# Kernel tuning notes

Measured on AMD Instinct MI355X. Metric: run time of the kernel, lower is better.

Reference implementation:

```python
import jax, jax.numpy as jnp
import numpy as np

N = 50000      # nodes per type
E = 800000     # edges per type (avg degree 16)
D = 128        # feature dim == hidden_channels
L = 3          # num_layers
G = 16         # graphs in batch
OUT = 2


def setup_inputs() -> dict:
    key = jax.random.key(0)
    ks = jax.random.split(key, 12)
    return {
        "x_void": jax.random.normal(ks[0], (N, D), jnp.float32),
        "x_vessel": jax.random.normal(ks[1], (N, D), jnp.float32),
        "Wl": jax.random.normal(ks[2], (L, 2, D, D), jnp.float32) * 0.05,
        "bl": jax.random.normal(ks[3], (L, 2, D), jnp.float32) * 0.05,
        "Wr": jax.random.normal(ks[4], (L, 2, D, D), jnp.float32) * 0.05,
        "lin_W": jax.random.normal(ks[5], (2 * D, OUT), jnp.float32) * 0.05,
        "lin_b": jax.random.normal(ks[6], (OUT,), jnp.float32) * 0.05,
        "edge_void": jax.random.randint(ks[7], (2, E), 0, N, jnp.int64 if jax.config.jax_enable_x64 else jnp.int32),
        "edge_vessel": jax.random.randint(ks[8], (2, E), 0, N, jnp.int64 if jax.config.jax_enable_x64 else jnp.int32),
        "batch_void": jnp.sort(jax.random.randint(ks[9], (N,), 0, G)),
        "batch_vessel": jnp.sort(jax.random.randint(ks[10], (N,), 0, G)),
    }


def _sage(x, src, dst, Wl_t, bl_t, Wr_t):
    # PyG SAGEConv (aggr='mean'): lin_l(mean_{j in N(i)} x_j) + lin_r(x_i)
    n = x.shape[0]
    agg = jax.ops.segment_sum(x[src], dst, num_segments=n)  # [n, D]
    cnt = jax.ops.segment_sum(jnp.ones((src.shape[0],), x.dtype), dst, num_segments=n)
    mean = agg / jnp.maximum(cnt, 1.0)[:, None]
    return mean @ Wl_t + bl_t + x @ Wr_t


def _mean_pool(x, batch, num_graphs):
    s = jax.ops.segment_sum(x, batch, num_segments=num_graphs)
    c = jax.ops.segment_sum(jnp.ones((x.shape[0],), x.dtype), batch, num_segments=num_graphs)
    return s / jnp.maximum(c, 1.0)[:, None]


def reference(x_void, x_vessel, Wl, bl, Wr, lin_W, lin_b,
              edge_void, edge_vessel, batch_void, batch_vessel):
    xs = [x_void, x_vessel]
    edges = [edge_void, edge_vessel]
    for l in range(L):
        xs = [jax.nn.relu(_sage(xs[t], edges[t][0], edges[t][1], Wl[l, t], bl[l, t], Wr[l, t]))
              for t in range(2)]
    reps = [_mean_pool(xs[0], batch_void, G), _mean_pool(xs[1], batch_vessel, G)]
    h = jnp.concatenate(reps, axis=1)  # [G, 2D]; dropout inactive (training=False)
    return h @ lin_W + lin_b
```

## Files before the change

kernel.cpp:

```cpp
#include <hip/hip_runtime.h>
#include <hip/hip_bf16.h>
#include <cstdint>
#include <cstddef>

static constexpr int FD = 128;
static constexpr int NG = 16;
static constexpr int NL = 3;

typedef __attribute__((ext_vector_type(8))) short short8;
typedef __attribute__((ext_vector_type(4))) float floatx4;

__device__ __forceinline__ short f2bf(float v) {
  union { __hip_bfloat16 b; short s; } u;
  u.b = __float2bfloat16(v);
  return u.s;
}
__device__ __forceinline__ float bfu(unsigned short u) {
  return __uint_as_float((unsigned int)u << 16);
}

__global__ __launch_bounds__(256) void k_bucket(
    const int* __restrict__ e0, const int* __restrict__ e1,
    int* __restrict__ gcount, int* __restrict__ buckets,
    int E, int NBUCK, int CAP)
{
  __shared__ int hist[256], lexcl[256], gbase[256], wcur[256];
  __shared__ int staged[4096];
  __shared__ int wsum[4];
  __shared__ int totalS;
  int tid = (int)threadIdx.x;
  int bx = (int)blockIdx.x;
  int t = bx & 1;
  int chunk = (bx >> 1) * 4096;
  const int* eg = t ? e1 : e0;
  hist[tid] = 0;
  __syncthreads();
  unsigned int ent[16];
  #pragma unroll
  for (int k = 0; k < 16; k++) {
    int i = chunk + k * 256 + tid;
    if (i < E) {
      unsigned int src = (unsigned int)eg[i];
      unsigned int dst = (unsigned int)eg[E + i];
      ent[k] = src | (dst << 16);
      atomicAdd(&hist[dst >> 8], 1);
    } else ent[k] = 0xFFFFFFFFu;
  }
  __syncthreads();
  int lane = tid & 63, wv = tid >> 6;
  int v = hist[tid];
  int sc = v;
  #pragma unroll
  for (int d = 1; d < 64; d <<= 1) {
    int tt = __shfl_up(sc, d, 64);
    if (lane >= d) sc += tt;
  }
  if (lane == 63) wsum[wv] = sc;
  __syncthreads();
  int wpre = 0;
  for (int w = 0; w < wv; w++) wpre += wsum[w];
  int excl = wpre + sc - v;
  lexcl[tid] = excl;
  wcur[tid] = excl;
  gbase[tid] = v ? atomicAdd(&gcount[t * 256 + tid], v) : 0;
  if (tid == 255) totalS = excl + v;
  __syncthreads();
  #pragma unroll
  for (int k = 0; k < 16; k++) {
    if (ent[k] != 0xFFFFFFFFu) {
      int b = ent[k] >> 24;
      int pos = atomicAdd(&wcur[b], 1);
      staged[pos] = (int)ent[k];
    }
  }
  __syncthreads();
  int total = totalS;
  for (int j = tid; j < total; j += 256) {
    unsigned int e = (unsigned int)staged[j];
    int b = e >> 24;
    int gp = gbase[b] + (j - lexcl[b]);
    if (gp < CAP) buckets[((size_t)t * NBUCK + b) * CAP + gp] = (int)e;
  }
}

__global__ __launch_bounds__(256) void k_csr(
    const int* __restrict__ gcount, const int* __restrict__ buckets,
    int* __restrict__ csr0, int* __restrict__ csr1,
    int* __restrict__ off0, int* __restrict__ off1,
    int* __restrict__ deg0, int* __restrict__ deg1,
    int NBUCK, int CAP, int n)
{
  __shared__ int hist[256], wcur[256], wsum[4];
  int tid = (int)threadIdx.x;
  int bx = (int)blockIdx.x;
  int t = bx & 1;
  int b = bx >> 1;
  int cnt = gcount[t * 256 + b];
  if (cnt > CAP) cnt = CAP;
  const int* base = buckets + ((size_t)t * NBUCK + b) * CAP;
  int* csr = t ? csr1 : csr0;
  int* off = t ? off1 : off0;
  int* deg = t ? deg1 : deg0;
  hist[tid] = 0;
  __syncthreads();
  for (int j = tid; j < cnt; j += 256)
    atomicAdd(&hist[((unsigned int)base[j] >> 16) & 255], 1);
  __syncthreads();
  int lane = tid & 63, wv = tid >> 6;
  int v = hist[tid];
  int sc = v;
  #pragma unroll
  for (int d = 1; d < 64; d <<= 1) {
    int tt = __shfl_up(sc, d, 64);
    if (lane >= d) sc += tt;
  }
  if (lane == 63) wsum[wv] = sc;
  __syncthreads();
  int wpre = 0;
  for (int w = 0; w < wv; w++) wpre += wsum[w];
  int excl = wpre + sc - v;
  wcur[tid] = excl;
  int node = b * 256 + tid;
  if (node < n) { deg[node] = v; off[node] = b * CAP + excl; }
  __syncthreads();
  for (int j = tid; j < cnt; j += 256) {
    unsigned int e = (unsigned int)base[j];
    int ld = (e >> 16) & 255;
    int pos = atomicAdd(&wcur[ld], 1);
    csr[b * CAP + pos] = (int)(e & 0xFFFFu);
  }
}

__global__ void k_wconv(const float* __restrict__ Wl, const float* __restrict__ Wr,
                        short* __restrict__ Wf) {
  int u = blockIdx.x * blockDim.x + threadIdx.x;
  if (u >= 6 * 8192) return;
  int combo = u >> 13;
  int r = u & 8191;
  int l  = r & 63;
  int nt = (r >> 6) & 7;
  int h  = (r >> 9) & 1;
  int ks = r >> 10;
  short8 s;
  #pragma unroll
  for (int j = 0; j < 8; j++) {
    int k = ks * 32 + (l >> 4) * 8 + j;
    int n = nt * 16 + (l & 15);
    float w = (k < FD) ? Wl[((size_t)combo * FD + k) * FD + n]
                       : Wr[((size_t)combo * FD + (k - FD)) * FD + n];
    __hip_bfloat16 hb = __float2bfloat16(w);
    if (h == 0) {
      union { __hip_bfloat16 b; short t; } uu; uu.b = hb; s[j] = uu.t;
    } else {
      float hf = __bfloat162float(hb);
      s[j] = f2bf(w - hf);
    }
  }
  *(short8*)(Wf + (size_t)combo * 65536 + (size_t)r * 8) = s;
}

__global__ __launch_bounds__(256) void k_xconv(
    const float* __restrict__ x0, const float* __restrict__ x1,
    short* __restrict__ a0, short* __restrict__ a1,
    short* __restrict__ r0, short* __restrict__ r1, int n) {
  int bx = blockIdx.x;
  int t = bx & 1;
  int g = bx >> 1;
  const float* x = t ? x1 : x0;
  short* a = t ? a1 : a0;
  short* rm = t ? r1 : r0;
  int tid = (int)threadIdx.x;
  int m = tid & 15;
  int kb = tid >> 4;
  int node = g * 16 + m;
  if (node >= n) return;
  const float* src = x + (size_t)node * FD + kb * 8;
  short8 s;
  #pragma unroll
  for (int j = 0; j < 8; j++) s[j] = f2bf(src[j]);
  *(short8*)(a + (size_t)g * 2048 + kb * 128 + m * 8) = s;
  *(short8*)(rm + (size_t)node * FD + kb * 8) = s;
}

__global__ __launch_bounds__(512) void k_agg(
    const unsigned short* __restrict__ x0, const unsigned short* __restrict__ x1,
    const int* __restrict__ csr0, const int* __restrict__ csr1,
    const int* __restrict__ off0, const int* __restrict__ off1,
    const int* __restrict__ deg0, const int* __restrict__ deg1,
    short* __restrict__ m0, short* __restrict__ m1, int n)
{
  __shared__ float M[16][132];
  int bx = blockIdx.x;
  int t = bx & 1;
  int g = bx >> 1;
  const unsigned short* x = t ? x1 : x0;
  const int* csr  = t ? csr1 : csr0;
  const int* off  = t ? off1 : off0;
  const int* deg  = t ? deg1 : deg0;
  short* mAF      = t ? m1 : m0;
  int tid = (int)threadIdx.x;
  int s = tid >> 5;
  int tx = tid & 31;
  int c4 = tx * 4;
  int node = g * 16 + s;
  if (node < n) {
    int o = off[node], d = deg[node];
    float a0 = 0.f, a1 = 0.f, a2 = 0.f, a3 = 0.f;
    for (int k0 = 0; k0 < d; k0 += 32) {
      int idx = (k0 + tx < d) ? csr[o + k0 + tx] : 0;
      int mm = min(32, d - k0);
      int j = 0;
      for (; j + 8 <= mm; j += 8) {
        int s0 = __shfl(idx, j + 0, 32);
        int s1 = __shfl(idx, j + 1, 32);
        int s2 = __shfl(idx, j + 2, 32);
        int s3 = __shfl(idx, j + 3, 32);
        int s4 = __shfl(idx, j + 4, 32);
        int s5 = __shfl(idx, j + 5, 32);
        int s6 = __shfl(idx, j + 6, 32);
        int s7 = __shfl(idx, j + 7, 32);
        ushort4 u0 = *(const ushort4*)&x[(size_t)s0 * FD + c4];
        ushort4 u1 = *(const ushort4*)&x[(size_t)s1 * FD + c4];
        ushort4 u2 = *(const ushort4*)&x[(size_t)s2 * FD + c4];
        ushort4 u3 = *(const ushort4*)&x[(size_t)s3 * FD + c4];
        ushort4 u4 = *(const ushort4*)&x[(size_t)s4 * FD + c4];
        ushort4 u5 = *(const ushort4*)&x[(size_t)s5 * FD + c4];
        ushort4 u6 = *(const ushort4*)&x[(size_t)s6 * FD + c4];
        ushort4 u7 = *(const ushort4*)&x[(size_t)s7 * FD + c4];
        a0 += ((bfu(u0.x) + bfu(u1.x)) + (bfu(u2.x) + bfu(u3.x)))
            + ((bfu(u4.x) + bfu(u5.x)) + (bfu(u6.x) + bfu(u7.x)));
        a1 += ((bfu(u0.y) + bfu(u1.y)) + (bfu(u2.y) + bfu(u3.y)))
            + ((bfu(u4.y) + bfu(u5.y)) + (bfu(u6.y) + bfu(u7.y)));
        a2 += ((bfu(u0.z) + bfu(u1.z)) + (bfu(u2.z) + bfu(u3.z)))
            + ((bfu(u4.z) + bfu(u5.z)) + (bfu(u6.z) + bfu(u7.z)));
        a3 += ((bfu(u0.w) + bfu(u1.w)) + (bfu(u2.w) + bfu(u3.w)))
            + ((bfu(u4.w) + bfu(u5.w)) + (bfu(u6.w) + bfu(u7.w)));
      }
      for (; j < mm; j++) {
        int si = __shfl(idx, j, 32);
        ushort4 u = *(const ushort4*)&x[(size_t)si * FD + c4];
        a0 += bfu(u.x); a1 += bfu(u.y); a2 += bfu(u.z); a3 += bfu(u.w);
      }
    }
    float inv = 1.f / fmaxf((float)d, 1.f);
    M[s][c4 + 0] = a0 * inv;
    M[s][c4 + 1] = a1 * inv;
    M[s][c4 + 2] = a2 * inv;
    M[s][c4 + 3] = a3 * inv;
  }
  __syncthreads();
  if (tid < 256) {
    int m = tid & 15;
    int kb = tid >> 4;
    if (g * 16 + m < n) {
      short8 v;
      #pragma unroll
      for (int j = 0; j < 8; j++) v[j] = f2bf(M[m][kb * 8 + j]);
      *(short8*)(mAF + (size_t)g * 2048 + kb * 128 + m * 8) = v;
    }
  }
}

__global__ __launch_bounds__(256) void k_gemm(
    const short* __restrict__ mAF0, const short* __restrict__ mAF1,
    const short* __restrict__ xAF0, const short* __restrict__ xAF1,
    const short* __restrict__ Wf,
    const float* __restrict__ bl,
    short* __restrict__ obf0, short* __restrict__ obf1,
    short* __restrict__ oAF0, short* __restrict__ oAF1, int n)
{
  __shared__ __align__(16) char smem[32768];
  short* WfL = (short*)smem;
  float* S   = (float*)smem;

  int tid = (int)threadIdx.x;
  int l = tid & 63;
  int wv = tid >> 6;
  int bx = (int)blockIdx.x;
  int t = bx & 1;
  int tile = bx >> 1;
  int row0 = tile * 128;
  int g0 = tile * 8;

  const short* mAF = t ? mAF1 : mAF0;
  const short* xAF = t ? xAF1 : xAF0;
  const short* Wc  = Wf + (size_t)t * 65536;
  const float* bias = bl + t * FD;
  short* obf = t ? obf1 : obf0;
  short* oAF = t ? oAF1 : oAF0;

  int rhalf = wv & 1;
  int chalf = wv >> 1;
  int laneoff = (l >> 4) * 128 + (l & 15) * 8;

  auto stageW = [&](int ks, int buf) {
    const short* src = Wc + ks * 8192 + wv * 2048;
    short* dst = WfL + buf * 8192 + wv * 2048;
    #pragma unroll
    for (int i = 0; i < 4; i++) {
      __builtin_amdgcn_global_load_lds(
          (const __attribute__((address_space(1))) void*)(src + i * 512 + l * 8),
          (__attribute__((address_space(3))) void*)(dst + i * 512),
          16, 0, 0);
    }
  };

  floatx4 acc[4][4];
  #pragma unroll
  for (int i = 0; i < 4; i++)
    #pragma unroll
    for (int q = 0; q < 4; q++) acc[i][q] = (floatx4)0.f;

  short8 Acur[4], Anext[4];
  auto loadA = [&](int ks, short8* A) {
    const short* Ab = (ks < 4 ? mAF : xAF) + (ks & 3) * 512;
    #pragma unroll
    for (int i = 0; i < 4; i++) {
      int g = g0 + rhalf * 4 + i;
      A[i] = *(const short8*)(Ab + (size_t)g * 2048 + laneoff);
    }
  };

  stageW(0, 0);
  loadA(0, Acur);
  for (int ks = 0; ks < 8; ks++) {
    int buf = ks & 1;
    __syncthreads();
    if (ks < 7) { stageW(ks + 1, buf ^ 1); loadA(ks + 1, Anext); }
    const short* WB = WfL + buf * 8192;
    #pragma unroll
    for (int q = 0; q < 4; q++) {
      int nt = chalf * 4 + q;
      short8 whi = *(const short8*)(WB + nt * 512 + l * 8);
      short8 wlo = *(const short8*)(WB + 4096 + nt * 512 + l * 8);
      #pragma unroll
      for (int i = 0; i < 4; i++) {
        acc[i][q] = __builtin_amdgcn_mfma_f32_16x16x32_bf16(Acur[i], whi, acc[i][q], 0, 0, 0);
        acc[i][q] = __builtin_amdgcn_mfma_f32_16x16x32_bf16(Acur[i], wlo, acc[i][q], 0, 0, 0);
      }
    }
    #pragma unroll
    for (int i = 0; i < 4; i++) Acur[i] = Anext[i];
  }

  #pragma unroll
  for (int q = 0; q < 4; q++) {
    int col = chalf * 64 + q * 16 + (l & 15);
    float b = bias[col];
    #pragma unroll
    for (int i = 0; i < 4; i++)
      #pragma unroll
      for (int r = 0; r < 4; r++)
        acc[i][q][r] = fmaxf(acc[i][q][r] + b, 0.f);
  }

  #pragma unroll
  for (int ph = 0; ph < 2; ph++) {
    __syncthreads();
    if (chalf == ph) {
      #pragma unroll
      for (int i = 0; i < 4; i++)
        #pragma unroll
        for (int q = 0; q < 4; q++)
          #pragma unroll
          for (int r = 0; r < 4; r++)
            S[(rhalf * 64 + i * 16 + (l >> 4) * 4 + r) * 64 + q * 16 + (l & 15)] = acc[i][q][r];
    }
    __syncthreads();
    #pragma unroll
    for (int it = 0; it < 4; it++) {
      int u = it * 256 + tid;
      int m = u & 15;
      int kb = (u >> 4) & 7;
      int grp = u >> 7;
      int rl = grp * 16 + m;
      if (row0 + rl < n) {
        short8 s;
        #pragma unroll
        for (int j = 0; j < 8; j++) s[j] = f2bf(S[rl * 64 + kb * 8 + j]);
        *(short8*)(oAF + (size_t)(g0 + grp) * 2048 + (ph * 8 + kb) * 128 + m * 8) = s;
        *(short8*)(obf + (size_t)(row0 + rl) * FD + ph * 64 + kb * 8) = s;
      }
    }
  }
}

__global__ __launch_bounds__(256) void k_pool(
    const unsigned short* __restrict__ x0, const unsigned short* __restrict__ x1,
    const int* __restrict__ b0, const int* __restrict__ b1,
    float* __restrict__ pool, float* __restrict__ pcnt, int n) {
  int bx = (int)blockIdx.x;
  int t = bx & 1;
  const unsigned short* x = t ? x1 : x0;
  const int* batch = t ? b1 : b0;
  float* pl = pool + t * NG * FD;
  float* pc = pcnt + t * NG;
  int tid = (int)threadIdx.x;
  int c4 = (tid & 31) * 4;
  int rs = tid >> 5;
  int start = (bx >> 1) * 128;
  int end = min(start + 128, n);
  if (start >= end) return;

  float4 acc = make_float4(0.f, 0.f, 0.f, 0.f);
  float cnt = 0.f;
  auto flush = [&](int g) {
    atomicAdd(&pl[g * FD + c4 + 0], acc.x);
    atomicAdd(&pl[g * FD + c4 + 1], acc.y);
    atomicAdd(&pl[g * FD + c4 + 2], acc.z);
    atomicAdd(&pl[g * FD + c4 + 3], acc.w);
    if ((tid & 31) == 0) atomicAdd(&pc[g], cnt);
  };

  int gfirst = batch[start];
  int glast = batch[end - 1];
  if (gfirst == glast) {
    for (int i = start + rs; i < end; i += 8) {
      ushort4 u = *(const ushort4*)&x[(size_t)i * FD + c4];
      acc.x += bfu(u.x); acc.y += bfu(u.y); acc.z += bfu(u.z); acc.w += bfu(u.w);
      cnt += 1.f;
    }
    flush(gfirst);
  } else {
    int curg = -1;
    for (int i = start + rs; i < end; i += 8) {
      int g = batch[i];
      if (g != curg) {
        if (curg >= 0) flush(curg);
        curg = g;
        acc = make_float4(0.f, 0.f, 0.f, 0.f);
        cnt = 0.f;
      }
      ushort4 u = *(const ushort4*)&x[(size_t)i * FD + c4];
      acc.x += bfu(u.x); acc.y += bfu(u.y); acc.z += bfu(u.z); acc.w += bfu(u.w);
      cnt += 1.f;
    }
    if (curg >= 0) flush(curg);
  }
}

__global__ void k_final(const float* __restrict__ pool, const float* __restrict__ pcnt,
                        const float* __restrict__ linW, const float* __restrict__ linb,
                        float* __restrict__ out) {
  int tid = (int)threadIdx.x;
  if (tid < NG * 2) {
    int g = tid >> 1, o = tid & 1;
    float s = linb[o];
    for (int t = 0; t < 2; t++) {
      float inv = 1.f / fmaxf(pcnt[t * NG + g], 1.f);
      for (int d = 0; d < FD; d++) {
        float h = pool[(t * NG + g) * FD + d] * inv;
        s = fmaf(h, linW[(t * FD + d) * 2 + o], s);
      }
    }
    out[g * 2 + o] = s;
  }
}

extern "C" void kernel_launch(void* const* d_in, const int* in_sizes, int n_in,
                              void* d_out, int out_size, void* d_ws, size_t ws_size,
                              hipStream_t stream) {
  const float* x_in[2] = {(const float*)d_in[0], (const float*)d_in[1]};
  const float* Wl   = (const float*)d_in[2];
  const float* bl   = (const float*)d_in[3];
  const float* Wr   = (const float*)d_in[4];
  const float* linW = (const float*)d_in[5];
  const float* linb = (const float*)d_in[6];
  const int* edges[2] = {(const int*)d_in[7], (const int*)d_in[8]};
  const int* batch[2] = {(const int*)d_in[9], (const int*)d_in[10]};

  const int N = in_sizes[0] / FD;
  const int E = in_sizes[7] / 2;
  const int NGRP = (N + 15) / 16;
  const int NTILE = (N + 127) / 128;
  const int NBUCK = (N + 255) / 256;
  const int CAP = 5120;
  const size_t AFG = (size_t)(NTILE * 8 + 8) * 2048;

  char* p = (char*)d_ws;
  auto alloc = [&](size_t bytes) -> char* {
    char* r = p; p += (bytes + 511) & ~(size_t)511; return r;
  };
  int* gcount  = (int*)alloc(2 * 256 * 4);
  float* pool  = (float*)alloc(2 * NG * FD * 4);
  float* pcnt  = (float*)alloc(2 * NG * 4);
  size_t zero_bytes = (size_t)(p - (char*)d_ws);
  int* off[2];  off[0]  = (int*)alloc((size_t)N * 4); off[1]  = (int*)alloc((size_t)N * 4);
  int* deg[2];  deg[0]  = (int*)alloc((size_t)N * 4); deg[1]  = (int*)alloc((size_t)N * 4);
  int* buckets = (int*)alloc((size_t)2 * NBUCK * CAP * 4);
  int* csr[2];  csr[0]  = (int*)alloc((size_t)NBUCK * CAP * 4);
                csr[1]  = (int*)alloc((size_t)NBUCK * CAP * 4);
  short* Wf    = (short*)alloc((size_t)6 * 65536 * 2);
  short* mAF[2]; mAF[0] = (short*)alloc(AFG * 2); mAF[1] = (short*)alloc(AFG * 2);
  short* xAF[2][2];
  for (int t = 0; t < 2; t++)
    for (int b = 0; b < 2; b++) xAF[t][b] = (short*)alloc(AFG * 2);
  short* xbf[2][2];
  for (int t = 0; t < 2; t++)
    for (int b = 0; b < 2; b++) xbf[t][b] = (short*)alloc((size_t)N * FD * 2);
  if ((size_t)(p - (char*)d_ws) > ws_size) return;

  hipMemsetAsync(d_ws, 0, zero_bytes, stream);

  k_wconv<<<(6 * 8192 + 255) / 256, 256, 0, stream>>>(Wl, Wr, Wf);
  k_xconv<<<2 * NGRP, 256, 0, stream>>>(x_in[0], x_in[1],
                                        xAF[0][0], xAF[1][0], xbf[0][0], xbf[1][0], N);
  int bblocks = 2 * ((E + 4095) / 4096);
  k_bucket<<<bblocks, 256, 0, stream>>>(edges[0], edges[1], gcount, buckets, E, NBUCK, CAP);
  k_csr<<<2 * NBUCK, 256, 0, stream>>>(gcount, buckets, csr[0], csr[1],
                                       off[0], off[1], deg[0], deg[1], NBUCK, CAP, N);

  int pp = 0;
  for (int l = 0; l < NL; l++) {
    k_agg<<<2 * NGRP, 512, 0, stream>>>(
        (const unsigned short*)xbf[0][pp], (const unsigned short*)xbf[1][pp],
        csr[0], csr[1], off[0], off[1], deg[0], deg[1], mAF[0], mAF[1], N);
    k_gemm<<<2 * NTILE, 256, 0, stream>>>(
        mAF[0], mAF[1], xAF[0][pp], xAF[1][pp],
        Wf + (size_t)l * 2 * 65536, bl + (size_t)l * 2 * FD,
        xbf[0][pp ^ 1], xbf[1][pp ^ 1], xAF[0][pp ^ 1], xAF[1][pp ^ 1], N);
    pp ^= 1;
  }

  int pblocks = 2 * ((N + 127) / 128);
  k_pool<<<pblocks, 256, 0, stream>>>(
      (const unsigned short*)xbf[0][pp], (const unsigned short*)xbf[1][pp],
      batch[0], batch[1], pool, pcnt, N);
  k_final<<<1, 64, 0, stream>>>(pool, pcnt, linW, linb, (float*)d_out);
}
```

Before: 467.8 us.

## Store CSR indices as 16-bit and make mean pooling a two-stage reduction

CSR neighbor indices (local node ids under 65536) are now stored as unsigned short, which halves the index traffic read by the aggregation kernel on every layer. Mean pooling is split into a per-chunk partial-sum kernel that reduces within a block through shared memory, then a second small kernel that combines the chunk partials per graph. This replaces many contended global atomics on 16 graph rows with a few, at the cost of an extra launch. The 16-bit CSR only holds while N fits in 16 bits.

```diff
diff --git a/kernel.cpp b/kernel.cpp
--- a/kernel.cpp
+++ b/kernel.cpp
@@ -85,7 +85,7 @@
 
 __global__ __launch_bounds__(256) void k_csr(
     const int* __restrict__ gcount, const int* __restrict__ buckets,
-    int* __restrict__ csr0, int* __restrict__ csr1,
+    unsigned short* __restrict__ csr0, unsigned short* __restrict__ csr1,
     int* __restrict__ off0, int* __restrict__ off1,
     int* __restrict__ deg0, int* __restrict__ deg1,
     int NBUCK, int CAP, int n)
@@ -98,7 +98,7 @@
   int cnt = gcount[t * 256 + b];
   if (cnt > CAP) cnt = CAP;
   const int* base = buckets + ((size_t)t * NBUCK + b) * CAP;
-  int* csr = t ? csr1 : csr0;
+  unsigned short* csr = t ? csr1 : csr0;
   int* off = t ? off1 : off0;
   int* deg = t ? deg1 : deg0;
   hist[tid] = 0;
@@ -127,7 +127,7 @@
     unsigned int e = (unsigned int)base[j];
     int ld = (e >> 16) & 255;
     int pos = atomicAdd(&wcur[ld], 1);
-    csr[b * CAP + pos] = (int)(e & 0xFFFFu);
+    csr[b * CAP + pos] = (unsigned short)(e & 0xFFFFu);
   }
 }
 
@@ -184,7 +184,7 @@
 
 __global__ __launch_bounds__(512) void k_agg(
     const unsigned short* __restrict__ x0, const unsigned short* __restrict__ x1,
-    const int* __restrict__ csr0, const int* __restrict__ csr1,
+    const unsigned short* __restrict__ csr0, const unsigned short* __restrict__ csr1,
     const int* __restrict__ off0, const int* __restrict__ off1,
     const int* __restrict__ deg0, const int* __restrict__ deg1,
     short* __restrict__ m0, short* __restrict__ m1, int n)
@@ -194,7 +194,7 @@
   int t = bx & 1;
   int g = bx >> 1;
   const unsigned short* x = t ? x1 : x0;
-  const int* csr  = t ? csr1 : csr0;
+  const unsigned short* csr = t ? csr1 : csr0;
   const int* off  = t ? off1 : off0;
   const int* deg  = t ? deg1 : deg0;
   short* mAF      = t ? m1 : m0;
@@ -207,7 +207,7 @@
     int o = off[node], d = deg[node];
     float a0 = 0.f, a1 = 0.f, a2 = 0.f, a3 = 0.f;
     for (int k0 = 0; k0 < d; k0 += 32) {
-      int idx = (k0 + tx < d) ? csr[o + k0 + tx] : 0;
+      int idx = (k0 + tx < d) ? (int)csr[o + k0 + tx] : 0;
       int mm = min(32, d - k0);
       int j = 0;
       for (; j + 8 <= mm; j += 8) {
@@ -385,57 +385,97 @@
   }
 }
 
-__global__ __launch_bounds__(256) void k_pool(
+__global__ __launch_bounds__(256) void k_pool1(
     const unsigned short* __restrict__ x0, const unsigned short* __restrict__ x1,
     const int* __restrict__ b0, const int* __restrict__ b1,
-    float* __restrict__ pool, float* __restrict__ pcnt, int n) {
+    float* __restrict__ part, int n, int NCH) {
+  __shared__ float R[8][128];
+  __shared__ int sb;
   int bx = (int)blockIdx.x;
   int t = bx & 1;
+  int ch = bx >> 1;
   const unsigned short* x = t ? x1 : x0;
   const int* batch = t ? b1 : b0;
+  float* P = part + ((size_t)t * NCH + ch) * 272;
+  int tid = (int)threadIdx.x;
+  int tx = tid & 31, rs = tid >> 5;
+  int c4 = tx * 4;
+  int start = ch * 128;
+  int end = min(start + 128, n);
+
+  int g0 = batch[start];
+  int g1 = batch[end - 1];
+  int lo[2], hi[2];
+  int nruns;
+  if (g0 == g1) {
+    lo[0] = start; hi[0] = end; nruns = 1;
+  } else {
+    if (tid == 0) sb = end;
+    __syncthreads();
+    for (int i = start + tid + 1; i < end; i += 256)
+      if (batch[i] != batch[i - 1]) atomicMin(&sb, i);
+    __syncthreads();
+    int b = sb;
+    lo[0] = start; hi[0] = b; lo[1] = b; hi[1] = end; nruns = 2;
+  }
+
+  for (int run = 0; run < nruns; run++) {
+    float4 a = make_float4(0.f, 0.f, 0.f, 0.f);
+    for (int i = lo[run] + rs; i < hi[run]; i += 8) {
+      ushort4 u = *(const ushort4*)&x[(size_t)i * FD + c4];
+      a.x += bfu(u.x); a.y += bfu(u.y); a.z += bfu(u.z); a.w += bfu(u.w);
+    }
+    *(float4*)&R[rs][c4] = a;
+    __syncthreads();
+    if (tid < 128) {
+      float s = 0.f;
+      #pragma unroll
+      for (int r = 0; r < 8; r++) s += R[r][tid];
+      P[run * 128 + tid] = s;
+    }
+    __syncthreads();
+  }
+  if (tid == 0) {
+    P[256] = (float)g0;
+    P[257] = (float)(hi[0] - lo[0]);
+    P[258] = (nruns == 2) ? (float)g1 : -1.f;
+    P[259] = (nruns == 2) ? (float)(hi[1] - lo[1]) : 0.f;
+  }
+}
+
+__global__ __launch_bounds__(128) void k_pool2(
+    const float* __restrict__ part, float* __restrict__ pool,
+    float* __restrict__ pcnt, int NCH, int CPS) {
+  int bx = (int)blockIdx.x;
+  int t = bx & 1;
+  int seg = bx >> 1;
+  int c0 = seg * CPS;
+  int c1 = min(c0 + CPS, NCH);
+  int tid = (int)threadIdx.x;
   float* pl = pool + t * NG * FD;
   float* pc = pcnt + t * NG;
-  int tid = (int)threadIdx.x;
-  int c4 = (tid & 31) * 4;
-  int rs = tid >> 5;
-  int start = (bx >> 1) * 128;
-  int end = min(start + 128, n);
-  if (start >= end) return;
-
-  float4 acc = make_float4(0.f, 0.f, 0.f, 0.f);
-  float cnt = 0.f;
-  auto flush = [&](int g) {
-    atomicAdd(&pl[g * FD + c4 + 0], acc.x);
-    atomicAdd(&pl[g * FD + c4 + 1], acc.y);
-    atomicAdd(&pl[g * FD + c4 + 2], acc.z);
-    atomicAdd(&pl[g * FD + c4 + 3], acc.w);
-    if ((tid & 31) == 0) atomicAdd(&pc[g], cnt);
-  };
-
-  int gfirst = batch[start];
-  int glast = batch[end - 1];
-  if (gfirst == glast) {
-    for (int i = start + rs; i < end; i += 8) {
-      ushort4 u = *(const ushort4*)&x[(size_t)i * FD + c4];
-      acc.x += bfu(u.x); acc.y += bfu(u.y); acc.z += bfu(u.z); acc.w += bfu(u.w);
-      cnt += 1.f;
-    }
-    flush(gfirst);
-  } else {
-    int curg = -1;
-    for (int i = start + rs; i < end; i += 8) {
-      int g = batch[i];
+  float acc = 0.f, ccnt = 0.f;
+  int curg = -1;
+  for (int ch = c0; ch < c1; ch++) {
+    const float* P = part + ((size_t)t * NCH + ch) * 272;
+    #pragma unroll
+    for (int r = 0; r < 2; r++) {
+      int g = (int)P[256 + r * 2];
+      if (g < 0) continue;
       if (g != curg) {
-        if (curg >= 0) flush(curg);
-        curg = g;
-        acc = make_float4(0.f, 0.f, 0.f, 0.f);
-        cnt = 0.f;
+        if (curg >= 0) {
+          atomicAdd(&pl[curg * FD + tid], acc);
+          if (tid == 0) atomicAdd(&pc[curg], ccnt);
+        }
+        curg = g; acc = 0.f; ccnt = 0.f;
       }
-      ushort4 u = *(const ushort4*)&x[(size_t)i * FD + c4];
-      acc.x += bfu(u.x); acc.y += bfu(u.y); acc.z += bfu(u.z); acc.w += bfu(u.w);
-      cnt += 1.f;
-    }
-    if (curg >= 0) flush(curg);
+      acc += P[r * 128 + tid];
+      if (tid == 0) ccnt += P[257 + r * 2];
+    }
+  }
+  if (curg >= 0) {
+    atomicAdd(&pl[curg * FD + tid], acc);
+    if (tid == 0) atomicAdd(&pc[curg], ccnt);
   }
 }
 
@@ -473,6 +513,7 @@
   const int E = in_sizes[7] / 2;
   const int NGRP = (N + 15) / 16;
   const int NTILE = (N + 127) / 128;
+  const int NCH = (N + 127) / 128;
   const int NBUCK = (N + 255) / 256;
   const int CAP = 5120;
   const size_t AFG = (size_t)(NTILE * 8 + 8) * 2048;
@@ -488,8 +529,10 @@
   int* off[2];  off[0]  = (int*)alloc((size_t)N * 4); off[1]  = (int*)alloc((size_t)N * 4);
   int* deg[2];  deg[0]  = (int*)alloc((size_t)N * 4); deg[1]  = (int*)alloc((size_t)N * 4);
   int* buckets = (int*)alloc((size_t)2 * NBUCK * CAP * 4);
-  int* csr[2];  csr[0]  = (int*)alloc((size_t)NBUCK * CAP * 4);
-                csr[1]  = (int*)alloc((size_t)NBUCK * CAP * 4);
+  unsigned short* csr[2];
+  csr[0] = (unsigned short*)alloc((size_t)NBUCK * CAP * 2);
+  csr[1] = (unsigned short*)alloc((size_t)NBUCK * CAP * 2);
+  float* part  = (float*)alloc((size_t)2 * NCH * 272 * 4);
   short* Wf    = (short*)alloc((size_t)6 * 65536 * 2);
   short* mAF[2]; mAF[0] = (short*)alloc(AFG * 2); mAF[1] = (short*)alloc(AFG * 2);
   short* xAF[2][2];
@@ -522,9 +565,10 @@
     pp ^= 1;
   }
 
-  int pblocks = 2 * ((N + 127) / 128);
-  k_pool<<<pblocks, 256, 0, stream>>>(
+  k_pool1<<<2 * NCH, 256, 0, stream>>>(
       (const unsigned short*)xbf[0][pp], (const unsigned short*)xbf[1][pp],
-      batch[0], batch[1], pool, pcnt, N);
+      batch[0], batch[1], part, N, NCH);
+  int CPS = (NCH + 7) / 8;
+  k_pool2<<<16, 128, 0, stream>>>(part, pool, pcnt, NCH, CPS);
   k_final<<<1, 64, 0, stream>>>(pool, pcnt, linW, linb, (float*)d_out);
 }
```

Result: faster. 447.8 us (-4.3%).
